# Optimization experiments

Measured on AMD Instinct MI355X. Metric: run time of the kernel, lower is better.

## Reference

```python
import jax, jax.numpy as jnp
import numpy as np

STRIDE = 2
F_SCALE = 4


def _layer_norm(x, eps=1e-5):
    # F.layer_norm over the last 3 dims (C,H,W), no affine
    m = jnp.mean(x, axis=(1, 2, 3), keepdims=True)
    v = jnp.var(x, axis=(1, 2, 3), keepdims=True)
    return (x - m) * jax.lax.rsqrt(v + eps)


def _conv(x, w, b, dil, pad):
    y = jax.lax.conv_general_dilated(
        x, w, window_strides=(1, 1), padding=[(pad, pad), (pad, pad)],
        rhs_dilation=(dil, dil), dimension_numbers=('NCHW', 'OIHW', 'NCHW'))
    return y + b[None, :, None, None]


def _unshuffle(x, f):
    # [B,C,H,W] -> [B*f*f, C, H/f, W/f]; sub-image k=dy*f+dx samples offsets (dy,dx) stride f
    B, C, H, W = x.shape
    sh, sw = H // f, W // f
    x = x.reshape(B, C, sh, f, sw, f)
    x = x.transpose(0, 3, 5, 1, 2, 4)  # [B, dy, dx, C, sh, sw]
    return x.reshape(B * f * f, C, sh, sw)


def _shuffle(x, B, f):
    # inverse of _unshuffle: [B*f*f, C, sh, sw] -> [B, C, sh*f, sw*f]
    _, C, sh, sw = x.shape
    x = x.reshape(B, f, f, C, sh, sw)
    x = x.transpose(0, 3, 4, 1, 5, 2)  # [B, C, sh, dy, sw, dx]
    return x.reshape(B, C, sh * f, sw * f)


def _attention(x, wqk, f):
    B, C, H, W = x.shape
    E = wqk.shape[1]
    ph, pw = (-H) % f, (-W) % f
    xx = _layer_norm(x)
    if ph or pw:
        xx = jnp.pad(xx, ((0, 0), (0, 0), (0, ph), (0, pw)))
        xp = jnp.pad(x, ((0, 0), (0, 0), (0, ph), (0, pw)))
    else:
        xp = x
    sub = _unshuffle(xx, f)   # [Bf, C, sh, sw]
    v = _unshuffle(xp, f)     # [Bf, C, sh, sw]
    Bf, _, sh, sw = sub.shape
    N = sh * sw
    q = sub.transpose(0, 2, 3, 1).reshape(Bf, N, C)
    vf = v.transpose(0, 2, 3, 1).reshape(Bf, N, C)
    qk = jnp.einsum('bnc,ce->bne', q, wqk)
    qk = qk / (jnp.linalg.norm(qk, axis=-1, keepdims=True) + 1e-8)
    attn = (jnp.einsum('bne,bme->bnm', qk, qk) + 1.0) / np.sqrt(E).astype(np.float32)
    attn = jax.nn.softmax(attn, axis=-1)
    out = jnp.einsum('bnm,bmc->bnc', attn, vf)
    out = out.reshape(Bf, sh, sw, C).transpose(0, 3, 1, 2)
    out = _shuffle(out, B, f)
    return out[:, :, :H, :W]


def setup_inputs() -> dict:
    key = jax.random.key(0)
    ks = jax.random.split(key, 8)
    B, C, H, W = 2, 128, 192, 192
    E = C  # ss_exp_factor = 1.0
    x = jax.random.normal(ks[0], (B, C, H, W), jnp.float32)
    lim = 1.414 * np.sqrt(6.0 / (C + E))  # xavier_uniform, gain=1.414
    wqk = jax.random.uniform(ks[1], (C, E), jnp.float32, -lim, lim)
    s = np.sqrt(2.0 / (C * 9)).astype(np.float32)
    w1 = jax.random.normal(ks[2], (C, C, 3, 3), jnp.float32) * s
    b1 = jnp.zeros((C,), jnp.float32)
    w2 = jax.random.normal(ks[3], (C, C, 3, 3), jnp.float32) * s
    b2 = jnp.zeros((C,), jnp.float32)
    w3 = jax.random.normal(ks[4], (C, C, 1, 1), jnp.float32) * np.sqrt(2.0 / C).astype(np.float32)
    b3 = jnp.zeros((C,), jnp.float32)
    return {"x": x, "wqk": wqk, "w1": w1, "b1": b1, "w2": w2, "b2": b2, "w3": w3, "b3": b3}


def reference(x, wqk, w1, b1, w2, b2, w3, b3):
    f = F_SCALE * STRIDE
    y = x + _attention(x, wqk, f)
    h = jax.nn.relu(_conv(y, w1, b1, STRIDE, STRIDE))
    h = jax.nn.relu(_conv(h, w2, b2, STRIDE, STRIDE))
    h = _conv(h, w3, b3, 1, 0)
    return x + h
```

## Files before the change

kernel.cpp:

```cpp
#include <hip/hip_runtime.h>
#include <math.h>

#define CCH 128
#define HH 192
#define WW 192
#define BB 2
#define HW (HH*WW)
#define CHW (CCH*HW)
#define BF 128
#define NN 576
#define SH 24

typedef __attribute__((ext_vector_type(8))) short short8;
typedef __attribute__((ext_vector_type(4))) float floatx4;
typedef unsigned int uint32;
typedef unsigned short ushort;

__device__ __forceinline__ unsigned short bf16r(float f) {
    uint32 u = __float_as_uint(f);
    u += 0x7fffu + ((u >> 16) & 1u);
    return (unsigned short)(u >> 16);
}

__global__ __launch_bounds__(256) void k_reduce(const float* __restrict__ x, float* __restrict__ stats) {
    int b = blockIdx.y;
    const float4* p = (const float4*)(x + (size_t)b*CHW) + (size_t)blockIdx.x*4096;
    float s = 0.f, sq = 0.f;
#pragma unroll
    for (int k = 0; k < 16; ++k) {
        float4 v = p[threadIdx.x + 256*k];
        s  += v.x + v.y + v.z + v.w;
        sq += v.x*v.x + v.y*v.y + v.z*v.z + v.w*v.w;
    }
    for (int off = 32; off; off >>= 1) { s += __shfl_down(s, off); sq += __shfl_down(sq, off); }
    __shared__ float ls[4], lq[4];
    int wave = threadIdx.x >> 6, lane = threadIdx.x & 63;
    if (lane == 0) { ls[wave] = s; lq[wave] = sq; }
    __syncthreads();
    if (threadIdx.x == 0) {
        atomicAdd(&stats[2*b],   ls[0]+ls[1]+ls[2]+ls[3]);
        atomicAdd(&stats[2*b+1], lq[0]+lq[1]+lq[2]+lq[3]);
    }
}

__global__ void k_finalize(float* stats) {
    int b = threadIdx.x;
    if (b < BB) {
        float s = stats[2*b], sq = stats[2*b+1];
        float mean = s / (float)CHW;
        float var = sq / (float)CHW - mean*mean;
        stats[4 + 2*b] = mean;
        stats[5 + 2*b] = rsqrtf(var + 1e-5f);
    }
}

__global__ __launch_bounds__(256) void k_unshuffle(const float* __restrict__ x, const float* __restrict__ stats,
                                                   ushort* __restrict__ Vt, ushort* __restrict__ Xnb) {
    __shared__ float t[128][65];
    int x0 = blockIdx.x * 64;
    int y  = blockIdx.y;
    int b  = blockIdx.z;
    float mean = stats[4+2*b], istd = stats[5+2*b];
    const float* src = x + (size_t)b*CHW + (size_t)y*WW + x0;
#pragma unroll
    for (int k = 0; k < 32; ++k) {
        int idx = threadIdx.x + 256*k;
        int c = idx >> 6, xl = idx & 63;
        t[c][xl] = src[(size_t)c*HW + xl];
    }
    __syncthreads();
    int i = y >> 3, dy = y & 7;
#pragma unroll
    for (int k = 0; k < 32; ++k) {
        int idx = threadIdx.x + 256*k;
        int xl = idx & 63, c = idx >> 6;
        int xx = x0 + xl;
        int j = xx >> 3, dx = xx & 7;
        int bf = (b << 6) + (dy << 3) + dx;
        int n = i*SH + j;
        Vt[((size_t)bf*CCH + c)*NN + n] = bf16r(t[c][xl]);
    }
#pragma unroll
    for (int k = 0; k < 16; ++k) {
        int idx = threadIdx.x + 256*k;
        int c2 = idx & 63, xl = idx >> 6;
        int c = c2 * 2;
        int xx = x0 + xl;
        int j = xx >> 3, dx = xx & 7;
        int bf = (b << 6) + (dy << 3) + dx;
        int n = i*SH + j;
        float v0 = (t[c][xl]   - mean) * istd;
        float v1 = (t[c+1][xl] - mean) * istd;
        uint32 p = (uint32)bf16r(v0) | ((uint32)bf16r(v1) << 16);
        *(uint32*)&Xnb[((size_t)bf*NN + n)*CCH + c] = p;
    }
}

__global__ __launch_bounds__(256) void k_qk(const ushort* __restrict__ Xnb, const ushort* __restrict__ wqkTb,
                                            ushort* __restrict__ qkn) {
    __shared__ ushort As[64*136];
    __shared__ ushort Bs[128*136];
    int bid = blockIdx.x;
    int bf = bid / 9, tile = bid % 9;
    int n0 = tile * 64;
    int tid = threadIdx.x;
    int wv = tid >> 6, l = tid & 63, quad = l >> 4, l15 = l & 15;
    {
        const uint4* asrc = (const uint4*)(Xnb + ((size_t)bf*NN + n0)*CCH);
        const uint4* bsrc = (const uint4*)wqkTb;
#pragma unroll
        for (int k = 0; k < 4; ++k) {
            int idx = tid + 256*k;
            int row = idx >> 4, co = idx & 15;
            *(uint4*)&As[row*136 + co*8] = asrc[idx];
        }
#pragma unroll
        for (int k = 0; k < 8; ++k) {
            int idx = tid + 256*k;
            int row = idx >> 4, co = idx & 15;
            *(uint4*)&Bs[row*136 + co*8] = bsrc[idx];
        }
    }
    __syncthreads();
    int qb = wv*16;
    short8 a[4];
#pragma unroll
    for (int kk = 0; kk < 4; ++kk)
        a[kk] = *(const short8*)&As[(qb + l15)*136 + kk*32 + quad*8];
    floatx4 acc[8];
#pragma unroll
    for (int nt = 0; nt < 8; ++nt) acc[nt] = (floatx4){0.f,0.f,0.f,0.f};
#pragma unroll
    for (int kk = 0; kk < 4; ++kk)
#pragma unroll
        for (int nt = 0; nt < 8; ++nt) {
            const short8 bfr = *(const short8*)&Bs[(nt*16 + l15)*136 + kk*32 + quad*8];
            acc[nt] = __builtin_amdgcn_mfma_f32_16x16x32_bf16(a[kk], bfr, acc[nt], 0, 0, 0);
        }
    float ss[4] = {0.f,0.f,0.f,0.f};
#pragma unroll
    for (int nt = 0; nt < 8; ++nt)
#pragma unroll
        for (int r = 0; r < 4; ++r) ss[r] += acc[nt][r]*acc[nt][r];
#pragma unroll
    for (int off = 1; off < 16; off <<= 1)
#pragma unroll
        for (int r = 0; r < 4; ++r) ss[r] += __shfl_xor(ss[r], off);
    float fr[4];
#pragma unroll
    for (int r = 0; r < 4; ++r) fr[r] = 1.f / (sqrtf(ss[r]) + 1e-8f);
    __syncthreads();
    ushort* mys = &As[qb*128];
#pragma unroll
    for (int nt = 0; nt < 8; ++nt)
#pragma unroll
        for (int r = 0; r < 4; ++r)
            mys[(quad*4 + r)*128 + nt*16 + l15] = bf16r(acc[nt][r]*fr[r]);
    uint4* dst = (uint4*)(qkn + ((size_t)bf*NN + n0 + qb)*CCH);
    const uint4* ls = (const uint4*)mys;
#pragma unroll
    for (int k = 0; k < 4; ++k)
        dst[l + 64*k] = ls[l + 64*k];
}

__global__ __launch_bounds__(256, 3) void k_attn(const ushort* __restrict__ qkn, const ushort* __restrict__ Vt_g,
                                                 float* __restrict__ O) {
    __shared__ ushort QPs[64*136];
    __shared__ ushort Ks[64*136];
    __shared__ ushort Vs[128*72];
    int id = blockIdx.x;
    int bfl = id & 7, widx = id >> 3;
    int tile = widx % 9;
    int bf = ((widx / 9) << 3) | bfl;
    int n0 = tile*64;
    int tid = threadIdx.x;
    int wv = tid >> 6, l = tid & 63, quad = l >> 4, l15 = l & 15;
    int qb = wv*16;

    const uint4* kv_base = (const uint4*)(qkn + (size_t)bf*NN*CCH);
    const uint4* vsrc = (const uint4*)(Vt_g + (size_t)bf*CCH*NN);

    {
        const uint4* qsrc = kv_base + (size_t)tile*1024;
#pragma unroll
        for (int k = 0; k < 4; ++k) {
            int idx = tid + 256*k;
            *(uint4*)&QPs[(idx >> 4)*136 + (idx & 15)*8] = qsrc[idx];
        }
    }
    __syncthreads();

    short8 aq[4];
#pragma unroll
    for (int kk = 0; kk < 4; ++kk)
        aq[kk] = *(const short8*)&QPs[(qb + l15)*136 + kk*32 + quad*8];

    floatx4 oacc[8];
#pragma unroll
    for (int ct = 0; ct < 8; ++ct) oacc[ct] = (floatx4){0.f,0.f,0.f,0.f};
    float rsum[4] = {0.f,0.f,0.f,0.f};
    const float scale = 0.08838834764831845f;
    ushort* Ps = QPs;

    for (int mt = 0; mt < 9; ++mt) {
        __syncthreads();
        {
            const uint4* ks = kv_base + (size_t)mt*1024;
            int mo8 = mt*8;
#pragma unroll
            for (int k = 0; k < 4; ++k) {
                int idx = tid + 256*k;
                *(uint4*)&Ks[(idx >> 4)*136 + (idx & 15)*8] = ks[idx];
            }
#pragma unroll
            for (int k = 0; k < 4; ++k) {
                int idx = tid + 256*k;
                *(uint4*)&Vs[(idx >> 3)*72 + (idx & 7)*8] = vsrc[(size_t)(idx >> 3)*72 + mo8 + (idx & 7)];
            }
        }
        __syncthreads();

        floatx4 sc[4];
#pragma unroll
        for (int t = 0; t < 4; ++t) sc[t] = (floatx4){0.f,0.f,0.f,0.f};
        __builtin_amdgcn_s_setprio(1);
#pragma unroll
        for (int kk = 0; kk < 4; ++kk)
#pragma unroll
            for (int t = 0; t < 4; ++t) {
                const short8 bk = *(const short8*)&Ks[(t*16 + l15)*136 + kk*32 + quad*8];
                sc[t] = __builtin_amdgcn_mfma_f32_16x16x32_bf16(aq[kk], bk, sc[t], 0, 0, 0);
            }
        __builtin_amdgcn_s_setprio(0);

        float pr[4] = {0.f,0.f,0.f,0.f};
#pragma unroll
        for (int t = 0; t < 4; ++t)
#pragma unroll
            for (int r = 0; r < 4; ++r) {
                float p = __expf((sc[t][r] + 1.f)*scale);
                Ps[(qb + quad*4 + r)*72 + t*16 + l15] = bf16r(p);
                pr[r] += p;
            }
#pragma unroll
        for (int off = 1; off < 16; off <<= 1)
#pragma unroll
            for (int r = 0; r < 4; ++r) pr[r] += __shfl_xor(pr[r], off);
#pragma unroll
        for (int r = 0; r < 4; ++r) rsum[r] += pr[r];

        short8 ap[2];
        ap[0] = *(const short8*)&Ps[(qb + l15)*72 + quad*8];
        ap[1] = *(const short8*)&Ps[(qb + l15)*72 + 32 + quad*8];
        __builtin_amdgcn_s_setprio(1);
#pragma unroll
        for (int ct = 0; ct < 8; ++ct)
#pragma unroll
            for (int kk2 = 0; kk2 < 2; ++kk2) {
                const short8 bv = *(const short8*)&Vs[(ct*16 + l15)*72 + kk2*32 + quad*8];
                oacc[ct] = __builtin_amdgcn_mfma_f32_16x16x32_bf16(ap[kk2], bv, oacc[ct], 0, 0, 0);
            }
        __builtin_amdgcn_s_setprio(0);
    }

    float rinv[4];
#pragma unroll
    for (int r = 0; r < 4; ++r) rinv[r] = 1.f / rsum[r];
#pragma unroll
    for (int ct = 0; ct < 8; ++ct)
#pragma unroll
        for (int r = 0; r < 4; ++r)
            O[((size_t)bf*NN + n0 + qb + quad*4 + r)*CCH + ct*16 + l15] = oacc[ct][r]*rinv[r];
}

__global__ __launch_bounds__(256) void k_shuffle_add(const float* __restrict__ O, const float* __restrict__ x,
                                                     uint4* __restrict__ yb) {
    __shared__ float t[128][65];
    int x0 = blockIdx.x * 64;
    int yy = blockIdx.y;
    int b  = blockIdx.z;
    if (blockIdx.x == 0 && threadIdx.x < 64) {
        int oct = threadIdx.x >> 2, p = threadIdx.x & 3;
        int col = (p < 2) ? p : 192 + p;
        uint4 z; z.x = 0; z.y = 0; z.z = 0; z.w = 0;
        yb[((size_t)(b*192 + yy)*16 + oct)*196 + col] = z;
    }
    int i = yy >> 3, dy = yy & 7;
#pragma unroll
    for (int k = 0; k < 32; ++k) {
        int idx = threadIdx.x + 256*k;
        int c = idx & 127, xl = idx >> 7;
        int xx = x0 + xl;
        int j = xx >> 3, dx = xx & 7;
        int bf = (b << 6) + (dy << 3) + dx;
        int n = i*SH + j;
        t[c][xl] = O[((size_t)bf*NN + n)*CCH + c];
    }
    __syncthreads();
    size_t base = (size_t)b*CHW + (size_t)yy*WW + x0;
#pragma unroll
    for (int k = 0; k < 32; ++k) {
        int idx = threadIdx.x + 256*k;
        int c = idx >> 6, xl = idx & 63;
        t[c][xl] += x[base + (size_t)c*HW + xl];
    }
    __syncthreads();
#pragma unroll
    for (int k = 0; k < 4; ++k) {
        int idx = threadIdx.x + 256*k;
        int xl = idx & 63, oc = idx >> 6;
        uint32 d[4];
#pragma unroll
        for (int j = 0; j < 4; ++j) {
            float f0 = t[oc*8 + 2*j][xl];
            float f1 = t[oc*8 + 2*j + 1][xl];
            d[j] = (uint32)bf16r(f0) | ((uint32)bf16r(f1) << 16);
        }
        uint4 v; v.x = d[0]; v.y = d[1]; v.z = d[2]; v.w = d[3];
        yb[((size_t)(b*192 + yy)*16 + oc)*196 + (x0 + xl + 2)] = v;
    }
}

__global__ __launch_bounds__(256) void k_cast_w(const float* __restrict__ w1, const float* __restrict__ w2,
                                                const float* __restrict__ w3, const float* __restrict__ wqk,
                                                uint4* __restrict__ wb1, uint4* __restrict__ wb2,
                                                uint4* __restrict__ w3b, uint4* __restrict__ wqkTb) {
    int id = blockIdx.x*256 + threadIdx.x;
    if (blockIdx.y == 2) {
        if (id < 2048) {
            int co = id >> 4, oct = id & 15;
            uint32 r[4];
#pragma unroll
            for (int j = 0; j < 4; ++j) {
                float f0 = w3[(size_t)co*128 + oct*8 + 2*j];
                float f1 = w3[(size_t)co*128 + oct*8 + 2*j + 1];
                r[j] = (uint32)bf16r(f0) | ((uint32)bf16r(f1) << 16);
            }
            uint4 v; v.x = r[0]; v.y = r[1]; v.z = r[2]; v.w = r[3];
            w3b[id] = v;
            int e = co;
            uint32 r2[4];
#pragma unroll
            for (int j = 0; j < 4; ++j) {
                float f0 = wqk[(size_t)(oct*8 + 2*j)*128 + e];
                float f1 = wqk[(size_t)(oct*8 + 2*j + 1)*128 + e];
                r2[j] = (uint32)bf16r(f0) | ((uint32)bf16r(f1) << 16);
            }
            uint4 v2; v2.x = r2[0]; v2.y = r2[1]; v2.z = r2[2]; v2.w = r2[3];
            wqkTb[id] = v2;
        }
        return;
    }
    const float* w = (blockIdx.y == 0) ? w1 : w2;
    uint4* wb = (blockIdx.y == 0) ? wb1 : wb2;
    int co = id & 127;
    int oct = (id >> 7) & 3;
    int chunk = (id >> 9) & 3;
    int tap = id >> 11;
    int ci0 = chunk*32 + oct*8;
    uint32 r[4];
#pragma unroll
    for (int j = 0; j < 4; ++j) {
        float f0 = w[(size_t)(co*128 + ci0 + 2*j)*9 + tap];
        float f1 = w[(size_t)(co*128 + ci0 + 2*j + 1)*9 + tap];
        r[j] = (uint32)bf16r(f0) | ((uint32)bf16r(f1) << 16);
    }
    uint4 v; v.x = r[0]; v.y = r[1]; v.z = r[2]; v.w = r[3];
    wb[((size_t)(tap*4 + chunk)*4 + oct)*128 + co] = v;
}

__global__ __launch_bounds__(256, 3) void k_conv3m(const uint4* __restrict__ yb, const uint4* __restrict__ wb,
                                                   const float* __restrict__ bias, void* __restrict__ outp,
                                                   int mode) {
    __shared__ uint4 As[864];
    __shared__ uint4 Ws[2][512];
    int xt = blockIdx.x;
    int rg = blockIdx.y;
    int b  = blockIdx.z;
    int par = rg & 1, g = rg >> 1;
    int y0 = 8*g + par;
    int x0 = xt*32;
    int tid = threadIdx.x;
    int wv = tid >> 6, l = tid & 63, quad = l >> 4, l15 = l & 15;
    int yw = y0 + 2*wv;

    if (mode == 0 && xt == 0) {
        int rowp = y0 + 2*(tid >> 6);
        int oct = (tid >> 2) & 15, p = tid & 3;
        int col = (p < 2) ? p : 192 + p;
        uint4 z; z.x = 0; z.y = 0; z.z = 0; z.w = 0;
        ((uint4*)outp)[((size_t)(b*192 + rowp)*16 + oct)*196 + col] = z;
    }

    floatx4 acc[2][8];
#pragma unroll
    for (int mt = 0; mt < 2; ++mt)
#pragma unroll
        for (int nt = 0; nt < 8; ++nt) acc[mt][nt] = (floatx4){0.f,0.f,0.f,0.f};

    const uint4* ybb = yb + (size_t)b*602112;

    for (int chunk = 0; chunk < 4; ++chunk) {
        __syncthreads();
#pragma unroll
        for (int k = 0; k < 4; ++k) {
            int idx = tid + 256*k;
            if (idx < 864) {
                int r = idx / 144;
                int rem = idx - r*144;
                int oct = rem / 36;
                int px = rem - oct*36;
                int grow = y0 - 2 + 2*r;
                uint4 v; v.x = 0; v.y = 0; v.z = 0; v.w = 0;
                if (grow >= 0 && grow < 192)
                    v = ybb[((size_t)grow*16 + chunk*4 + oct)*196 + x0 + px];
                As[idx] = v;
            }
        }
        {
            const uint4* src = wb + (size_t)chunk*512;
            Ws[0][tid]     = src[tid];
            Ws[0][tid+256] = src[tid+256];
        }
        __syncthreads();
#pragma unroll
        for (int tap = 0; tap < 9; ++tap) {
            if (tap < 8) {
                const uint4* src = wb + (size_t)((tap+1)*4 + chunk)*512;
                Ws[(tap+1)&1][tid]     = src[tid];
                Ws[(tap+1)&1][tid+256] = src[tid+256];
            }
            const int ky = tap/3, kx = tap - 3*(tap/3);
            int r = wv + ky;
            const short8 a0 = *(const short8*)&As[(r*4 + quad)*36 + l15 + 2*kx];
            const short8 a1 = *(const short8*)&As[(r*4 + quad)*36 + 16 + l15 + 2*kx];
            const uint4* wbuf = &Ws[tap&1][0];
#pragma unroll
            for (int nt = 0; nt < 8; ++nt) {
                const short8 bf = *(const short8*)&wbuf[quad*128 + nt*16 + l15];
                acc[0][nt] = __builtin_amdgcn_mfma_f32_16x16x32_bf16(a0, bf, acc[0][nt], 0, 0, 0);
                acc[1][nt] = __builtin_amdgcn_mfma_f32_16x16x32_bf16(a1, bf, acc[1][nt], 0, 0, 0);
            }
            __syncthreads();
        }
    }

    if (mode == 0) {
        unsigned short* outb = (unsigned short*)outp;
#pragma unroll
        for (int nt = 0; nt < 8; ++nt) {
            int co = nt*16 + l15;
            float bv = bias[co];
            size_t base = (((size_t)(b*192 + yw)*16 + ((co>>5)*4 + ((co>>3)&3)))*196)*8 + (size_t)(co&7);
#pragma unroll
            for (int mt = 0; mt < 2; ++mt)
#pragma unroll
                for (int rr = 0; rr < 4; ++rr) {
                    int xx = x0 + mt*16 + quad*4 + rr;
                    float v = fmaxf(acc[mt][nt][rr] + bv, 0.f);
                    outb[base + (size_t)(xx+2)*8] = bf16r(v);
                }
        }
    } else {
        unsigned short* outb = (unsigned short*)outp;
#pragma unroll
        for (int nt = 0; nt < 8; ++nt) {
            int co = nt*16 + l15;
            float bv = bias[co];
#pragma unroll
            for (int mt = 0; mt < 2; ++mt)
#pragma unroll
                for (int rr = 0; rr < 4; ++rr) {
                    int xx = x0 + mt*16 + quad*4 + rr;
                    float v = fmaxf(acc[mt][nt][rr] + bv, 0.f);
                    outb[((size_t)b*36864 + (size_t)yw*192 + xx)*128 + co] = bf16r(v);
                }
        }
    }
}

__global__ __launch_bounds__(256, 2) void k_conv1x1m(const ushort* __restrict__ h2b, const uint4* __restrict__ w3b,
                                                     const float* __restrict__ b3, const float* __restrict__ x,
                                                     float* __restrict__ out) {
    __shared__ ushort Hs[128*136];
    __shared__ ushort Ws3[128*136];
    int px0 = blockIdx.x * 128;
    int b = blockIdx.y;
    int tid = threadIdx.x;
    int wv = tid >> 6, l = tid & 63, quad = l >> 4, l15 = l & 15;

    {
        const uint4* hsrc = (const uint4*)(h2b + ((size_t)b*36864 + px0)*128);
#pragma unroll
        for (int k = 0; k < 8; ++k) {
            int idx = tid + 256*k;
            int row = idx >> 4, co8 = idx & 15;
            *(uint4*)&Hs[row*136 + co8*8] = hsrc[idx];
            *(uint4*)&Ws3[row*136 + co8*8] = w3b[idx];
        }
    }
    __syncthreads();

    floatx4 oacc[2][8];
#pragma unroll
    for (int mt = 0; mt < 2; ++mt)
#pragma unroll
        for (int nt = 0; nt < 8; ++nt) oacc[mt][nt] = (floatx4){0.f,0.f,0.f,0.f};

#pragma unroll
    for (int kk = 0; kk < 4; ++kk) {
        const short8 aq0 = *(const short8*)&Hs[(wv*32 + l15)*136 + kk*32 + quad*8];
        const short8 aq1 = *(const short8*)&Hs[(wv*32 + 16 + l15)*136 + kk*32 + quad*8];
#pragma unroll
        for (int nt = 0; nt < 8; ++nt) {
            const short8 bw = *(const short8*)&Ws3[(nt*16 + l15)*136 + kk*32 + quad*8];
            oacc[0][nt] = __builtin_amdgcn_mfma_f32_16x16x32_bf16(aq0, bw, oacc[0][nt], 0, 0, 0);
            oacc[1][nt] = __builtin_amdgcn_mfma_f32_16x16x32_bf16(aq1, bw, oacc[1][nt], 0, 0, 0);
        }
    }

#pragma unroll
    for (int nt = 0; nt < 8; ++nt) {
        int co = nt*16 + l15;
        float bv = b3[co];
        size_t pbase = ((size_t)b*128 + co)*HW + px0 + wv*32 + quad*4;
#pragma unroll
        for (int mt = 0; mt < 2; ++mt) {
            const float4 xv = *(const float4*)&x[pbase + mt*16];
            float4 o;
            o.x = oacc[mt][nt][0] + bv + xv.x;
            o.y = oacc[mt][nt][1] + bv + xv.y;
            o.z = oacc[mt][nt][2] + bv + xv.z;
            o.w = oacc[mt][nt][3] + bv + xv.w;
            *(float4*)&out[pbase + mt*16] = o;
        }
    }
}

extern "C" void kernel_launch(void* const* d_in, const int* in_sizes, int n_in,
                              void* d_out, int out_size, void* d_ws, size_t ws_size,
                              hipStream_t stream) {
    (void)in_sizes; (void)n_in; (void)out_size; (void)ws_size;
    const float* x   = (const float*)d_in[0];
    const float* wqk = (const float*)d_in[1];
    const float* w1  = (const float*)d_in[2];
    const float* b1  = (const float*)d_in[3];
    const float* w2  = (const float*)d_in[4];
    const float* b2  = (const float*)d_in[5];
    const float* w3  = (const float*)d_in[6];
    const float* b3  = (const float*)d_in[7];
    float* out = (float*)d_out;
    char* ws = (char*)d_ws;
    float* stats = (float*)ws;
    const size_t SZ = (size_t)BF * NN * CCH * sizeof(float);
    char* Abase = ws + 256;
    char* Bbase = ws + 256 + SZ;
    char* Cbase = ws + 256 + 2*SZ;
    ushort* Vt  = (ushort*)Abase;
    ushort* Xnb = (ushort*)Bbase;
    ushort* qkn = (ushort*)Cbase;
    float*  O   = (float*)Bbase;
    uint4*  yb  = (uint4*)Cbase;
    uint4*  h1b = (uint4*)Abase;
    ushort* h2b = (ushort*)Bbase;
    uint4* wb1   = (uint4*)(Abase + 20*1024*1024);
    uint4* wb2   = (uint4*)(Abase + 21*1024*1024);
    uint4* w3b   = (uint4*)(Abase + 22*1024*1024);
    uint4* wqkTb = (uint4*)(Abase + 23*1024*1024);

    hipMemsetAsync(stats, 0, 4*sizeof(float), stream);
    k_reduce     <<<dim3(288, 2),     256, 0, stream>>>(x, stats);
    k_finalize   <<<1, 64,            0, stream>>>(stats);
    k_cast_w     <<<dim3(72, 3),      256, 0, stream>>>(w1, w2, w3, wqk, wb1, wb2, w3b, wqkTb);
    k_unshuffle  <<<dim3(3, 192, 2),  256, 0, stream>>>(x, stats, Vt, Xnb);
    k_qk         <<<1152,             256, 0, stream>>>(Xnb, (const ushort*)wqkTb, qkn);
    k_attn       <<<1152,             256, 0, stream>>>(qkn, Vt, O);
    k_shuffle_add<<<dim3(3, 192, 2),  256, 0, stream>>>(O, x, yb);
    k_conv3m     <<<dim3(6, 48, 2),   256, 0, stream>>>(yb,  wb1, b1, (void*)h1b, 0);
    k_conv3m     <<<dim3(6, 48, 2),   256, 0, stream>>>(h1b, wb2, b2, (void*)h2b, 1);
    k_conv1x1m   <<<dim3(288, 2),     256, 0, stream>>>(h2b, w3b, b3, x, out);
}
```

Baseline: 298.1 us.

## Load Q fragments from global directly and enlarge attention query tile to 96 rows

In both the QK projection and the attention kernels, A/Q fragments are now read directly from global memory into registers instead of being staged through shared memory. That removes one LDS buffer and one barrier per kernel. The attention kernel now uses 384 threads (6 waves) covering 96 query rows per block, launched as 768 blocks. This lets each K/V tile load into shared memory be reused by more queries, cutting total K/V traffic, and the P buffer stride is padded to 76. The trade-off is uncoalesced-ish per-lane global reads for Q and predicated cooperative loads, plus different occupancy from the new launch bounds.

```diff
diff --git a/kernel.cpp b/kernel.cpp
--- a/kernel.cpp
+++ b/kernel.cpp
@@ -96,9 +96,8 @@
     }
 }
 
-__global__ __launch_bounds__(256) void k_qk(const ushort* __restrict__ Xnb, const ushort* __restrict__ wqkTb,
-                                            ushort* __restrict__ qkn) {
-    __shared__ ushort As[64*136];
+__global__ __launch_bounds__(256, 4) void k_qk(const ushort* __restrict__ Xnb, const ushort* __restrict__ wqkTb,
+                                               ushort* __restrict__ qkn) {
     __shared__ ushort Bs[128*136];
     int bid = blockIdx.x;
     int bf = bid / 9, tile = bid % 9;
@@ -106,14 +105,7 @@
     int tid = threadIdx.x;
     int wv = tid >> 6, l = tid & 63, quad = l >> 4, l15 = l & 15;
     {
-        const uint4* asrc = (const uint4*)(Xnb + ((size_t)bf*NN + n0)*CCH);
         const uint4* bsrc = (const uint4*)wqkTb;
-#pragma unroll
-        for (int k = 0; k < 4; ++k) {
-            int idx = tid + 256*k;
-            int row = idx >> 4, co = idx & 15;
-            *(uint4*)&As[row*136 + co*8] = asrc[idx];
-        }
 #pragma unroll
         for (int k = 0; k < 8; ++k) {
             int idx = tid + 256*k;
@@ -121,12 +113,13 @@
             *(uint4*)&Bs[row*136 + co*8] = bsrc[idx];
         }
     }
-    __syncthreads();
     int qb = wv*16;
+    const ushort* arow = Xnb + ((size_t)bf*NN + n0 + qb + l15)*CCH + quad*8;
     short8 a[4];
 #pragma unroll
     for (int kk = 0; kk < 4; ++kk)
-        a[kk] = *(const short8*)&As[(qb + l15)*136 + kk*32 + quad*8];
+        a[kk] = *(const short8*)(arow + kk*32);
+    __syncthreads();
     floatx4 acc[8];
 #pragma unroll
     for (int nt = 0; nt < 8; ++nt) acc[nt] = (floatx4){0.f,0.f,0.f,0.f};
@@ -150,7 +143,7 @@
 #pragma unroll
     for (int r = 0; r < 4; ++r) fr[r] = 1.f / (sqrtf(ss[r]) + 1e-8f);
     __syncthreads();
-    ushort* mys = &As[qb*128];
+    ushort* mys = &Bs[qb*128];
 #pragma unroll
     for (int nt = 0; nt < 8; ++nt)
 #pragma unroll
@@ -163,16 +156,16 @@
         dst[l + 64*k] = ls[l + 64*k];
 }
 
-__global__ __launch_bounds__(256, 3) void k_attn(const ushort* __restrict__ qkn, const ushort* __restrict__ Vt_g,
+__global__ __launch_bounds__(384, 4) void k_attn(const ushort* __restrict__ qkn, const ushort* __restrict__ Vt_g,
                                                  float* __restrict__ O) {
-    __shared__ ushort QPs[64*136];
     __shared__ ushort Ks[64*136];
     __shared__ ushort Vs[128*72];
+    __shared__ ushort Ps[96*76];
     int id = blockIdx.x;
     int bfl = id & 7, widx = id >> 3;
-    int tile = widx % 9;
-    int bf = ((widx / 9) << 3) | bfl;
-    int n0 = tile*64;
+    int tile = widx % 6;
+    int bf = ((widx / 6) << 3) | bfl;
+    int n0 = tile*96;
     int tid = threadIdx.x;
     int wv = tid >> 6, l = tid & 63, quad = l >> 4, l15 = l & 15;
     int qb = wv*16;
@@ -180,27 +173,17 @@
     const uint4* kv_base = (const uint4*)(qkn + (size_t)bf*NN*CCH);
     const uint4* vsrc = (const uint4*)(Vt_g + (size_t)bf*CCH*NN);
 
-    {
-        const uint4* qsrc = kv_base + (size_t)tile*1024;
-#pragma unroll
-        for (int k = 0; k < 4; ++k) {
-            int idx = tid + 256*k;
-            *(uint4*)&QPs[(idx >> 4)*136 + (idx & 15)*8] = qsrc[idx];
-        }
-    }
-    __syncthreads();
-
+    const ushort* qrow = qkn + ((size_t)bf*NN + n0 + qb + l15)*CCH + quad*8;
     short8 aq[4];
 #pragma unroll
     for (int kk = 0; kk < 4; ++kk)
-        aq[kk] = *(const short8*)&QPs[(qb + l15)*136 + kk*32 + quad*8];
+        aq[kk] = *(const short8*)(qrow + kk*32);
 
     floatx4 oacc[8];
 #pragma unroll
     for (int ct = 0; ct < 8; ++ct) oacc[ct] = (floatx4){0.f,0.f,0.f,0.f};
     float rsum[4] = {0.f,0.f,0.f,0.f};
     const float scale = 0.08838834764831845f;
-    ushort* Ps = QPs;
 
     for (int mt = 0; mt < 9; ++mt) {
         __syncthreads();
@@ -208,14 +191,16 @@
             const uint4* ks = kv_base + (size_t)mt*1024;
             int mo8 = mt*8;
 #pragma unroll
-            for (int k = 0; k < 4; ++k) {
-                int idx = tid + 256*k;
-                *(uint4*)&Ks[(idx >> 4)*136 + (idx & 15)*8] = ks[idx];
-            }
-#pragma unroll
-            for (int k = 0; k < 4; ++k) {
-                int idx = tid + 256*k;
-                *(uint4*)&Vs[(idx >> 3)*72 + (idx & 7)*8] = vsrc[(size_t)(idx >> 3)*72 + mo8 + (idx & 7)];
+            for (int k = 0; k < 3; ++k) {
+                int idx = tid + 384*k;
+                if (idx < 1024)
+                    *(uint4*)&Ks[(idx >> 4)*136 + (idx & 15)*8] = ks[idx];
+            }
+#pragma unroll
+            for (int k = 0; k < 3; ++k) {
+                int idx = tid + 384*k;
+                if (idx < 1024)
+                    *(uint4*)&Vs[(idx >> 3)*72 + (idx & 7)*8] = vsrc[(size_t)(idx >> 3)*72 + mo8 + (idx & 7)];
             }
         }
         __syncthreads();
@@ -239,7 +224,7 @@
 #pragma unroll
             for (int r = 0; r < 4; ++r) {
                 float p = __expf((sc[t][r] + 1.f)*scale);
-                Ps[(qb + quad*4 + r)*72 + t*16 + l15] = bf16r(p);
+                Ps[(qb + quad*4 + r)*76 + t*16 + l15] = bf16r(p);
                 pr[r] += p;
             }
 #pragma unroll
@@ -250,8 +235,8 @@
         for (int r = 0; r < 4; ++r) rsum[r] += pr[r];
 
         short8 ap[2];
-        ap[0] = *(const short8*)&Ps[(qb + l15)*72 + quad*8];
-        ap[1] = *(const short8*)&Ps[(qb + l15)*72 + 32 + quad*8];
+        ap[0] = *(const short8*)&Ps[(qb + l15)*76 + quad*8];
+        ap[1] = *(const short8*)&Ps[(qb + l15)*76 + 32 + quad*8];
         __builtin_amdgcn_s_setprio(1);
 #pragma unroll
         for (int ct = 0; ct < 8; ++ct)
@@ -574,7 +559,7 @@
     k_cast_w     <<<dim3(72, 3),      256, 0, stream>>>(w1, w2, w3, wqk, wb1, wb2, w3b, wqkTb);
     k_unshuffle  <<<dim3(3, 192, 2),  256, 0, stream>>>(x, stats, Vt, Xnb);
     k_qk         <<<1152,             256, 0, stream>>>(Xnb, (const ushort*)wqkTb, qkn);
-    k_attn       <<<1152,             256, 0, stream>>>(qkn, Vt, O);
+    k_attn       <<<768,              384, 0, stream>>>(qkn, Vt, O);
     k_shuffle_add<<<dim3(3, 192, 2),  256, 0, stream>>>(O, x, yb);
     k_conv3m     <<<dim3(6, 48, 2),   256, 0, stream>>>(yb,  wb1, b1, (void*)h1b, 0);
     k_conv3m     <<<dim3(6, 48, 2),   256, 0, stream>>>(h1b, wb2, b2, (void*)h2b, 1);
```

After: 311.9 us. 1.05x slower.
